# Kernel optimization log

Hardware: AMD Instinct MI355X
Metric: run time of the kernel (lower is better)

The kernel has to match this reference:

```python
import jax, jax.numpy as jnp
import numpy as np
import math

DIM = 96
NUM_HEADS = 8
MLP_RATIO = 4.0

def _coord_encoding(h, w, scale, d_model):
    # matches HierarchicalCoordinateEncoding: per freq i, channels are
    # [sin(cell_y), cos(cell_y), sin(cell_x), cos(cell_x), sin(y), cos(y), sin(x), cos(x)]
    y = jnp.arange(h, dtype=jnp.float32) / (h - 1)
    x = jnp.arange(w, dtype=jnp.float32) / (w - 1)
    yy, xx = jnp.meshgrid(y, x, indexing='ij')
    yf = yy.reshape(-1)
    xf = xx.reshape(-1)
    cs = 2.0 / scale
    coords4 = jnp.stack([yf * cs, xf * cs, yf, xf], axis=-1)  # [N,4]
    nf = d_model // 8
    freqs = (2.0 ** jnp.arange(nf, dtype=jnp.float32)) * math.pi  # [nf]
    phase = coords4[:, None, :] * freqs[None, :, None]  # [N,nf,4]
    enc = jnp.stack([jnp.sin(phase), jnp.cos(phase)], axis=-1)  # [N,nf,4,2]
    return enc.reshape(h * w, nf * 8)  # [N,d_model] (d_model divisible by 8)

def _layernorm(x, g, b, eps=1e-5):
    mu = jnp.mean(x, axis=-1, keepdims=True)
    var = jnp.var(x, axis=-1, keepdims=True)
    return (x - mu) * jax.lax.rsqrt(var + eps) * g + b

def setup_inputs():
    key = jax.random.key(0)
    ks = jax.random.split(key, 8)
    B, C, H, W = 8, DIM, 96, 96
    hid = int(DIM * MLP_RATIO)
    std = 0.02
    return {
        'features': jax.random.normal(ks[0], (B, C, H, W), jnp.float32),
        'scale': 2,
        'mlp1_w1': jax.random.normal(ks[1], (2 * DIM, hid), jnp.float32) * std,
        'mlp1_b1': jnp.zeros((hid,), jnp.float32),
        'mlp1_w2': jax.random.normal(ks[2], (hid, DIM), jnp.float32) * std,
        'mlp1_b2': jnp.zeros((DIM,), jnp.float32),
        'norm1_g': jnp.ones((DIM,), jnp.float32),
        'norm1_b': jnp.zeros((DIM,), jnp.float32),
        'qkv_w': jax.random.normal(ks[3], (DIM, 3 * DIM), jnp.float32) * std,
        'proj_w': jax.random.normal(ks[4], (DIM, DIM), jnp.float32) * std,
        'proj_b': jnp.zeros((DIM,), jnp.float32),
        'norm2_g': jnp.ones((DIM,), jnp.float32),
        'norm2_b': jnp.zeros((DIM,), jnp.float32),
        'mlp2_w1': jax.random.normal(ks[5], (DIM, hid), jnp.float32) * std,
        'mlp2_b1': jnp.zeros((hid,), jnp.float32),
        'mlp2_w2': jax.random.normal(ks[6], (hid, 3), jnp.float32) * std,
        'mlp2_b2': jnp.zeros((3,), jnp.float32),
    }

def reference(features, scale, mlp1_w1, mlp1_b1, mlp1_w2, mlp1_b2, norm1_g, norm1_b, qkv_w, proj_w, proj_b, norm2_g, norm2_b, mlp2_w1, mlp2_b1, mlp2_w2, mlp2_b2):
    B, C, H_lr, W_lr = features.shape
    H, W = int(H_lr * scale), int(W_lr * scale)
    N = H * W
    nh = NUM_HEADS
    hd = C // nh
    ce = _coord_encoding(H, W, float(scale), C)  # [N,C]
    # bilinear upsample, half-pixel centers == torch align_corners=False
    feat_up = jax.image.resize(features, (B, C, H, W), method='linear')
    feat_flat = feat_up.transpose(0, 2, 3, 1).reshape(B, N, C)
    combined = jnp.concatenate([feat_flat, jnp.broadcast_to(ce[None], (B, N, C))], axis=-1)  # [B,N,2C]
    x = jax.nn.gelu(combined @ mlp1_w1 + mlp1_b1, approximate=False) @ mlp1_w2 + mlp1_b2  # [B,N,C]
    x = _layernorm(x, norm1_g, norm1_b)
    # linear attention: softmax over q feature dim and k token dim
    qkv = (x @ qkv_w).reshape(B, N, 3, nh, hd).transpose(2, 0, 3, 1, 4)  # [3,B,nh,N,hd]
    q, k, v = qkv[0], qkv[1], qkv[2]
    q = jax.nn.softmax(q, axis=-1) * (hd ** -0.5)
    k = jax.nn.softmax(k, axis=-2)
    ctx = jnp.einsum('bhnd,bhne->bhde', k, v)  # [B,nh,hd,hd]
    attn = jnp.einsum('bhnd,bhde->bhne', q, ctx)  # [B,nh,N,hd]
    attn = attn.transpose(0, 2, 1, 3).reshape(B, N, C)
    x = x + (attn @ proj_w + proj_b)
    x = _layernorm(x, norm2_g, norm2_b)
    rgb = jax.nn.gelu(x @ mlp2_w1 + mlp2_b1, approximate=False) @ mlp2_w2 + mlp2_b2  # [B,N,3]
    rgb = rgb.reshape(B, H, W, 3).transpose(0, 3, 1, 2)  # [B,3,H,W]
    return jnp.clip(jnp.tanh(rgb) * 0.5 + 0.5, 0.0, 1.0)
```

## Files before the change

kernel.cpp:

```cpp
#include <hip/hip_runtime.h>
#include <math.h>

typedef unsigned short u16;
typedef unsigned int   u32;
typedef unsigned long long u64;
typedef __bf16  bf16x8 __attribute__((ext_vector_type(8)));
typedef short   s16x8  __attribute__((ext_vector_type(8)));
typedef float   f32x4  __attribute__((ext_vector_type(4)));

#define NTOK 36864
#define TTOT (8*NTOK)

__device__ __forceinline__ f32x4 mfma16(s16x8 a, s16x8 b, f32x4 c){
  return __builtin_amdgcn_mfma_f32_16x16x32_bf16(
      __builtin_bit_cast(bf16x8, a), __builtin_bit_cast(bf16x8, b), c, 0, 0, 0);
}
__device__ __forceinline__ int swz(int row, int bc, int stride){
  return row*stride + (bc ^ ((row&7)<<4));
}
__device__ __forceinline__ u16 f2bf(float f){
  u32 u = __float_as_uint(f);
  return (u16)((u + 0x7fffu + ((u>>16)&1u)) >> 16);
}
__device__ __forceinline__ u32 pk2f(float a, float b){
  return (u32)f2bf(a) | ((u32)f2bf(b)<<16);
}
__device__ __forceinline__ u64 pk4f(float a, float b, float c, float d){
  return (u64)pk2f(a,b) | ((u64)pk2f(c,d)<<32);
}
__device__ __forceinline__ float bf2f(u16 h){ return __uint_as_float(((u32)h)<<16); }
__device__ __forceinline__ float rcp_(float x){ return __builtin_amdgcn_rcpf(x); }

__device__ __forceinline__ float gelu_(float x){
  float z = fabsf(x) * 0.70710678118654752f;
  float t = rcp_(1.0f + 0.3275911f*z);
  float poly = t*(0.254829592f + t*(-0.284496736f + t*(1.421413741f + t*(-1.453152027f + t*1.061405429f))));
  float e = __expf(-z*z);
  float erf = 1.0f - poly*e;
  erf = (x < 0.0f) ? -erf : erf;
  return 0.5f*x*(1.0f + erf);
}
__device__ __forceinline__ float tanhf_(float x){
  float e = __expf(2.0f*x);
  return 1.0f - 2.0f*rcp_(e + 1.0f);
}

#define LDSF(arr, row, kc, stride) (*(const s16x8*)((const char*)(arr) + swz((row),(kc)*2,(stride))))

__global__ void prep_w(const float* __restrict__ w1, const float* __restrict__ w2,
                       const float* __restrict__ qkvw, const float* __restrict__ projw,
                       const float* __restrict__ m2w1, const float* __restrict__ m2w2,
                       u16* __restrict__ w1t, u16* __restrict__ w2t,
                       u16* __restrict__ wqt, u16* __restrict__ wkt, u16* __restrict__ wvt,
                       u16* __restrict__ pjt, u16* __restrict__ m2w1t, u16* __restrict__ m2w2t)
{
  int i = blockIdx.x*256 + threadIdx.x;
  if (i < 73728){ int n=i/192, k=i%192; w1t[i] = f2bf(w1[k*384+n]); return; }
  i -= 73728;
  if (i < 36864){ int n=i/384, k=i%384; w2t[i] = f2bf(w2[k*96+n]); return; }
  i -= 36864;
  if (i < 9216){ int n=i/96, k=i%96; wqt[i] = f2bf(qkvw[k*288+n]); return; }
  i -= 9216;
  if (i < 9216){ int n=i/96, k=i%96; wkt[i] = f2bf(qkvw[k*288+96+n]); return; }
  i -= 9216;
  if (i < 9216){ int n=i/96, k=i%96; wvt[i] = f2bf(qkvw[k*288+192+n]); return; }
  i -= 9216;
  if (i < 9216){ int n=i/96, k=i%96; pjt[i] = f2bf(projw[k*96+n]); return; }
  i -= 9216;
  if (i < 36864){ int n=i/96, k=i%96; m2w1t[i] = f2bf(m2w1[k*384+n]); return; }
  i -= 36864;
  if (i < 6144){ int n=i/384, k=i%384; m2w2t[i] = (n<3)? f2bf(m2w2[k*3+n]) : (u16)0; return; }
}

__global__ void prep_feat(const float* __restrict__ feat, u16* __restrict__ featcl){
  __shared__ u16 t[96*100];
  const int tid = threadIdx.x;
  const int b = blockIdx.x/96, y = blockIdx.x%96;
  for (int i=tid; i<9216; i+=256){
    int c = i/96, x = i%96;
    t[c*100+x] = f2bf(feat[((size_t)(b*96+c)*96 + y)*96 + x]);
  }
  __syncthreads();
  for (int i=tid; i<9216; i+=256){
    int x = i/96, c = i%96;
    featcl[(((size_t)b*96 + y)*96 + x)*96 + c] = t[c*100+x];
  }
}

__global__ void prep_ce(u16* __restrict__ ce){
  int gid = blockIdx.x*256 + threadIdx.x;
  if (gid >= 36864*48) return;
  int n = gid/48, c2 = gid%48;
  int row = n/192, col = n%192;
  int fi = c2>>2, cs = c2&3;
  float coord = ((cs&1)==0) ? (float)row*(1.0f/191.0f) : (float)col*(1.0f/191.0f);
  float u = coord * (float)(1<<fi);
  u = u - 2.0f*floorf(u*0.5f);
  float ph = u * 3.14159265358979323846f;
  float s, c;
  __sincosf(ph, &s, &c);
  *(u32*)(ce + (size_t)n*96 + c2*2) = pk2f(s, c);
}

__global__ __launch_bounds__(256,3) void k1(
    const u16* __restrict__ featcl, const u16* __restrict__ ce,
    const u16* __restrict__ w1t, const float* __restrict__ b1,
    const u16* __restrict__ w2t, const float* __restrict__ b2,
    const float* __restrict__ g1, const float* __restrict__ be1,
    const u16* __restrict__ wkt, const u16* __restrict__ wvt,
    u16* __restrict__ x1, float* __restrict__ ctx_un)
{
  __shared__ u16 comb[64*192];
  __shared__ char scratch[26624];
  const int tid = threadIdx.x, w = tid>>6, lane = tid&63, kg = lane>>4, ln = lane&15;
  const int bi = blockIdx.x;
  const int b = bi/576, rem = bi%576, ty = rem/24, tx = rem%24;
  u16* hid  = (u16*)scratch;
  u16* ektp = (u16*)scratch;
  u16* vtp  = (u16*)(scratch + 12288);

  for (int i=tid; i<1024; i+=256){
    int rr = 96 + (i>>6), t = i&63;
    *(u16*)((char*)vtp + swz(rr, t*2, 128)) = (rr==96) ? (u16)0x3f80 : (u16)0;
  }

  {
    const u16* fbase = featcl + (size_t)b*884736;
    const int l = tid>>2, cg = tid&3;
    int row = ty*8 + (l>>3), col = tx*8 + (l&7);
    int y0 = (row-1)>>1;
    int y0c = max(y0,0), y1c = min(y0+1,95);
    float wy1 = (row&1) ? 0.25f : 0.75f;
    float wy0 = 1.0f - wy1;
    int x0 = (col-1)>>1;
    int x0c = max(x0,0), x1c = min(x0+1,95);
    float wx1 = (col&1) ? 0.25f : 0.75f;
    float wx0 = 1.0f - wx1;
    float w00=wy0*wx0, w01=wy0*wx1, w10=wy1*wx0, w11=wy1*wx1;
    const u16* p00 = fbase + (size_t)(y0c*96+x0c)*96 + cg*24;
    const u16* p01 = fbase + (size_t)(y0c*96+x1c)*96 + cg*24;
    const u16* p10 = fbase + (size_t)(y1c*96+x0c)*96 + cg*24;
    const u16* p11 = fbase + (size_t)(y1c*96+x1c)*96 + cg*24;
    #pragma unroll
    for (int g=0; g<3; ++g){
      s16x8 v00 = *(const s16x8*)(p00 + g*8);
      s16x8 v01 = *(const s16x8*)(p01 + g*8);
      s16x8 v10 = *(const s16x8*)(p10 + g*8);
      s16x8 v11 = *(const s16x8*)(p11 + g*8);
      #pragma unroll
      for (int j2=0; j2<4; ++j2){
        u32 u00 = ((const u32*)&v00)[j2], u01 = ((const u32*)&v01)[j2];
        u32 u10 = ((const u32*)&v10)[j2], u11 = ((const u32*)&v11)[j2];
        float a0 = w00*bf2f((u16)u00) + w01*bf2f((u16)u01)
                 + w10*bf2f((u16)u10) + w11*bf2f((u16)u11);
        float a1 = w00*bf2f((u16)(u00>>16)) + w01*bf2f((u16)(u01>>16))
                 + w10*bf2f((u16)(u10>>16)) + w11*bf2f((u16)(u11>>16));
        *(u32*)((char*)comb + swz(l, (cg*24 + g*8 + j2*2)*2, 384)) = pk2f(a0, a1);
      }
    }
  }
  for (int i=tid; i<64*12; i+=256){
    int l = i/12, sg = i%12;
    int n = (ty*8+(l>>3))*192 + tx*8 + (l&7);
    *(s16x8*)((char*)comb + swz(l, 192 + sg*16, 384)) = *(const s16x8*)(ce + (size_t)n*96 + sg*8);
  }
  __syncthreads();

  f32x4 a2[6] = {};
  for (int h=0; h<2; ++h){
    f32x4 acc[3][4] = {};
    #pragma unroll
    for (int ks=0; ks<6; ++ks){
      s16x8 af[3];
      #pragma unroll
      for (int nf=0; nf<3; ++nf)
        af[nf] = *(const s16x8*)(w1t + (size_t)(192*h+48*w+16*nf+ln)*192 + ks*32+8*kg);
      #pragma unroll
      for (int tf=0; tf<4; ++tf){
        s16x8 bfr = LDSF(comb, 16*tf+ln, ks*32+8*kg, 384);
        #pragma unroll
        for (int nf=0; nf<3; ++nf) acc[nf][tf] = mfma16(af[nf], bfr, acc[nf][tf]);
      }
    }
    #pragma unroll
    for (int nf=0; nf<3; ++nf){
      int lc0 = 48*w + 16*nf + 4*kg;
      float4 bb = *(const float4*)(b1 + 192*h + lc0);
      #pragma unroll
      for (int tf=0; tf<4; ++tf){
        int token = 16*tf + ln;
        u64 v = pk4f(gelu_(acc[nf][tf][0]+bb.x), gelu_(acc[nf][tf][1]+bb.y),
                     gelu_(acc[nf][tf][2]+bb.z), gelu_(acc[nf][tf][3]+bb.w));
        *(u64*)((char*)hid + swz(token, lc0*2, 384)) = v;
      }
    }
    __syncthreads();
    #pragma unroll
    for (int ks=0; ks<6; ++ks){
      s16x8 af = LDSF(hid, 16*w+ln, ks*32+8*kg, 384);
      #pragma unroll
      for (int nf=0; nf<6; ++nf){
        s16x8 bfr = *(const s16x8*)(w2t + (size_t)(16*nf+ln)*384 + 192*h + ks*32+8*kg);
        a2[nf] = mfma16(af, bfr, a2[nf]);
      }
    }
    if (h==0) __syncthreads();
  }

  float gg[6], bbv[6];
  #pragma unroll
  for (int nf=0; nf<6; ++nf){
    int col = 16*nf + ln;
    float bias = b2[col];
    gg[nf] = g1[col]; bbv[nf] = be1[col];
    #pragma unroll
    for (int r=0; r<4; ++r) a2[nf][r] += bias;
  }
  __syncthreads();
  #pragma unroll
  for (int r=0; r<4; ++r){
    float s=0.f, sq=0.f;
    #pragma unroll
    for (int nf=0; nf<6; ++nf){ float v=a2[nf][r]; s+=v; sq+=v*v; }
    #pragma unroll
    for (int m=8; m; m>>=1){ s += __shfl_xor(s,m); sq += __shfl_xor(sq,m); }
    float mean = s*(1.f/96.f);
    float var  = sq*(1.f/96.f) - mean*mean;
    float rstd = rsqrtf(var + 1e-5f);
    int trow = 16*w + 4*kg + r;
    #pragma unroll
    for (int nf=0; nf<6; ++nf){
      float o = (a2[nf][r]-mean)*rstd*gg[nf] + bbv[nf];
      *(u16*)((char*)comb + swz(trow, (16*nf+ln)*2, 256)) = f2bf(o);
    }
  }
  __syncthreads();

  for (int i=tid; i<64*12; i+=256){
    int l = i/12, sg = i%12;
    s16x8 v = *(const s16x8*)((const char*)comb + swz(l, sg*16, 256));
    int n = (ty*8+(l>>3))*192 + tx*8 + (l&7);
    *(s16x8*)(x1 + ((size_t)b*NTOK + n)*96 + sg*8) = v;
  }

  {
    f32x4 ka[6] = {}, va[6] = {};
    #pragma unroll
    for (int ks=0; ks<3; ++ks){
      s16x8 xb = LDSF(comb, 16*w+ln, ks*32+8*kg, 256);
      #pragma unroll
      for (int mf=0; mf<6; ++mf){
        s16x8 ak = *(const s16x8*)(wkt + (size_t)(16*mf+ln)*96 + ks*32+8*kg);
        s16x8 av = *(const s16x8*)(wvt + (size_t)(16*mf+ln)*96 + ks*32+8*kg);
        ka[mf] = mfma16(ak, xb, ka[mf]);
        va[mf] = mfma16(av, xb, va[mf]);
      }
    }
    #pragma unroll
    for (int mf=0; mf<6; ++mf){
      #pragma unroll
      for (int r=0; r<4; ++r){
        int d = 16*mf + 4*kg + r;
        int tok = 16*w + ln;
        *(u16*)((char*)ektp + swz(d, tok*2, 128)) = f2bf(__expf(ka[mf][r]));
        *(u16*)((char*)vtp  + swz(d, tok*2, 128)) = f2bf(va[mf][r]);
      }
    }
  }
  __syncthreads();

  {
    const int tmi[20] = {0,0,1,1,1,2,2,3,3,4,4,4,5,5, 0,1,2,3,4,5};
    const int tni[20] = {0,1,0,1,2,1,2,3,4,3,4,5,4,5, 6,6,6,6,6,6};
    f32x4 c5[5] = {};
    #pragma unroll
    for (int t=0; t<20; ++t){
      if (t/5 == w){
        #pragma unroll
        for (int grp=0; grp<2; ++grp){
          s16x8 ea = LDSF(ektp, 16*tmi[t]+ln, 32*grp+8*kg, 128);
          s16x8 vb = LDSF(vtp,  16*tni[t]+ln, 32*grp+8*kg, 128);
          c5[t%5] = mfma16(ea, vb, c5[t%5]);
        }
      }
    }
    #pragma unroll
    for (int t=0; t<20; ++t){
      if (t/5 == w){
        #pragma unroll
        for (int r=0; r<4; ++r){
          int d = 16*tmi[t] + 4*kg + r;
          if (tni[t]==6){
            if (ln==0) atomicAdd(&ctx_un[(b*96+d)*112 + 96], c5[t%5][r]);
          } else {
            int e = 16*tni[t] + ln;
            if (d/12 == e/12) atomicAdd(&ctx_un[(b*96+d)*112 + e], c5[t%5][r]);
          }
        }
      }
    }
  }
}

__global__ void k2c(const float* __restrict__ ctx_un, u16* __restrict__ ctxBG){
  int i = blockIdx.x*256 + threadIdx.x;
  if (i >= 8*112*128) return;
  int b = i/14336, rr = i%14336, row = rr/128, d = rr%128;
  u16 v = 0;
  if (row < 96){
    if (d < 96 && d/12 == row/12){
      float c = ctx_un[(b*96+d)*112 + row] / ctx_un[(b*96+d)*112 + 96];
      v = f2bf(c * 0.28867513459481287f);
    }
  } else {
    int h = row - 96;
    if (d < 96 && d/12 == h) v = (u16)0x3f80;
  }
  ctxBG[(size_t)b*14336 + row*128 + d] = v;
}

__global__ __launch_bounds__(256,2) void k3(
    const u16* __restrict__ x1, const u16* __restrict__ wqt, const u16* __restrict__ ctxBG,
    const u16* __restrict__ pjt,
    const float* __restrict__ projb, const float* __restrict__ g2, const float* __restrict__ be2,
    const u16* __restrict__ m2w1t, const float* __restrict__ m2b1,
    const u16* __restrict__ m2w2t, const float* __restrict__ m2b2,
    float* __restrict__ out)
{
  __shared__ u16 bufA[128*128];
  __shared__ u16 bufB[128*128];
  __shared__ float rgbsh[3][128];
  const int tid = threadIdx.x, w = tid>>6, lane = tid&63, kg = lane>>4, ln = lane&15;
  const int bi = blockIdx.x, b = bi/288;
  const size_t t0 = (size_t)bi*128;
  const int n0 = (bi%288)*128;

  {
    s16x8 wq[18], xbv[6];
    #pragma unroll
    for (int ks=0; ks<3; ++ks)
      #pragma unroll
      for (int nf=0; nf<6; ++nf)
        wq[ks*6+nf] = *(const s16x8*)(wqt + (size_t)(16*nf+ln)*96 + ks*32+8*kg);
    #pragma unroll
    for (int tf=0; tf<2; ++tf)
      #pragma unroll
      for (int ks=0; ks<3; ++ks)
        xbv[tf*3+ks] = *(const s16x8*)(x1 + (t0 + 32*w + 16*tf + ln)*96 + ks*32+8*kg);
    f32x4 q[6][2] = {};
    #pragma unroll
    for (int ks=0; ks<3; ++ks)
      #pragma unroll
      for (int tf=0; tf<2; ++tf)
        #pragma unroll
        for (int nf=0; nf<6; ++nf)
          q[nf][tf] = mfma16(wq[ks*6+nf], xbv[tf*3+ks], q[nf][tf]);
    #pragma unroll
    for (int nf=0; nf<6; ++nf){
      #pragma unroll
      for (int tf=0; tf<2; ++tf){
        int token = 32*w + 16*tf + ln;
        u64 v = pk4f(__expf(q[nf][tf][0]), __expf(q[nf][tf][1]),
                     __expf(q[nf][tf][2]), __expf(q[nf][tf][3]));
        *(u64*)((char*)bufA + swz(token, (16*nf+4*kg)*2, 256)) = v;
      }
    }
  }

  f32x4 p[2][7] = {};
  {
    const u16* cb = ctxBG + (size_t)b*14336;
    s16x8 cbf[21];
    #pragma unroll
    for (int ks=0; ks<3; ++ks)
      #pragma unroll
      for (int nf=0; nf<7; ++nf)
        cbf[ks*7+nf] = *(const s16x8*)(cb + (size_t)(16*nf+ln)*128 + ks*32+8*kg);
    #pragma unroll
    for (int ks=0; ks<3; ++ks){
      s16x8 a[2];
      #pragma unroll
      for (int mi=0; mi<2; ++mi) a[mi] = LDSF(bufA, 16*(2*w+mi)+ln, ks*32+8*kg, 256);
      #pragma unroll
      for (int nf=0; nf<7; ++nf){
        #pragma unroll
        for (int mi=0; mi<2; ++mi) p[mi][nf] = mfma16(a[mi], cbf[ks*7+nf], p[mi][nf]);
      }
    }
  }
  f32x4 pp[2][6];
  #pragma unroll
  for (int mi=0; mi<2; ++mi)
    #pragma unroll
    for (int nf=0; nf<6; ++nf)
      #pragma unroll
      for (int r=0; r<4; ++r)
        pp[mi][nf][r] = bf2f(x1[(t0 + 16*(2*w+mi)+4*kg+r)*96 + 16*nf+ln]);
  s16x8 pjf[18];
  #pragma unroll
  for (int ks=0; ks<3; ++ks)
    #pragma unroll
    for (int nf=0; nf<6; ++nf)
      pjf[ks*6+nf] = *(const s16x8*)(pjt + (size_t)(16*nf+ln)*96 + ks*32+8*kg);
  #pragma unroll
  for (int mi=0; mi<2; ++mi){
    f32x4 inv;
    #pragma unroll
    for (int r=0; r<4; ++r) inv[r] = rcp_(p[mi][6][r]);
    #pragma unroll
    for (int nf=0; nf<6; ++nf){
      int h = (16*nf + ln) / 12;
      int src = (lane & 0x30) + h;
      #pragma unroll
      for (int r=0; r<4; ++r){
        float iv = __shfl(inv[r], src, 64);
        int trow = 16*(2*w+mi) + 4*kg + r;
        *(u16*)((char*)bufB + swz(trow, (16*nf+ln)*2, 256)) = f2bf(p[mi][nf][r] * iv);
      }
    }
  }

  #pragma unroll
  for (int ks=0; ks<3; ++ks){
    s16x8 a[2];
    #pragma unroll
    for (int mi=0; mi<2; ++mi) a[mi] = LDSF(bufB, 16*(2*w+mi)+ln, ks*32+8*kg, 256);
    #pragma unroll
    for (int nf=0; nf<6; ++nf){
      #pragma unroll
      for (int mi=0; mi<2; ++mi) pp[mi][nf] = mfma16(a[mi], pjf[ks*6+nf], pp[mi][nf]);
    }
  }
  {
    float gg[6], bbv[6], pb[6];
    #pragma unroll
    for (int nf=0; nf<6; ++nf){
      int col = 16*nf + ln;
      pb[nf] = projb[col]; gg[nf] = g2[col]; bbv[nf] = be2[col];
    }
    #pragma unroll
    for (int mi=0; mi<2; ++mi){
      #pragma unroll
      for (int r=0; r<4; ++r){
        int trow = 16*(2*w+mi)+4*kg+r;
        float vv[6]; float s=0.f, sq=0.f;
        #pragma unroll
        for (int nf=0; nf<6; ++nf){
          float v = pp[mi][nf][r] + pb[nf];
          vv[nf] = v; s += v; sq += v*v;
        }
        #pragma unroll
        for (int m=8; m; m>>=1){ s += __shfl_xor(s,m); sq += __shfl_xor(sq,m); }
        float mean = s*(1.f/96.f);
        float var  = sq*(1.f/96.f) - mean*mean;
        float rstd = rsqrtf(var + 1e-5f);
        #pragma unroll
        for (int nf=0; nf<6; ++nf){
          float o = (vv[nf]-mean)*rstd*gg[nf] + bbv[nf];
          *(u16*)((char*)bufA + swz(trow, (16*nf+ln)*2, 256)) = f2bf(o);
        }
      }
    }
  }

  f32x4 rgb[2] = {};
  for (int nc=0; nc<4; ++nc){
    s16x8 wm[18];
    #pragma unroll
    for (int ks=0; ks<3; ++ks)
      #pragma unroll
      for (int nf=0; nf<6; ++nf)
        wm[ks*6+nf] = *(const s16x8*)(m2w1t + (size_t)(nc*96+16*nf+ln)*96 + ks*32+8*kg);
    s16x8 wv2[3];
    #pragma unroll
    for (int ks=0; ks<3; ++ks)
      wv2[ks] = *(const s16x8*)(m2w2t + (size_t)ln*384 + nc*96 + ks*32 + 8*kg);
    f32x4 hh[6][2] = {};
    #pragma unroll
    for (int ks=0; ks<3; ++ks){
      #pragma unroll
      for (int tf=0; tf<2; ++tf){
        s16x8 bfr = LDSF(bufA, 32*w+16*tf+ln, ks*32+8*kg, 256);
        #pragma unroll
        for (int nf=0; nf<6; ++nf) hh[nf][tf] = mfma16(wm[ks*6+nf], bfr, hh[nf][tf]);
      }
    }
    #pragma unroll
    for (int nf=0; nf<6; ++nf){
      int hc0 = nc*96 + 16*nf + 4*kg;
      float4 bb = *(const float4*)(m2b1 + hc0);
      #pragma unroll
      for (int tf=0; tf<2; ++tf){
        int token = 32*w + 16*tf + ln;
        u64 v = pk4f(gelu_(hh[nf][tf][0]+bb.x), gelu_(hh[nf][tf][1]+bb.y),
                     gelu_(hh[nf][tf][2]+bb.z), gelu_(hh[nf][tf][3]+bb.w));
        *(u64*)((char*)bufB + swz(token, (16*nf+4*kg)*2, 256)) = v;
      }
    }
    #pragma unroll
    for (int ks=0; ks<3; ++ks){
      #pragma unroll
      for (int mi=0; mi<2; ++mi){
        s16x8 a = LDSF(bufB, 16*(2*w+mi)+ln, ks*32+8*kg, 256);
        rgb[mi] = mfma16(a, wv2[ks], rgb[mi]);
      }
    }
  }
  if (ln < 3){
    float bias = m2b2[ln];
    #pragma unroll
    for (int mi=0; mi<2; ++mi)
      #pragma unroll
      for (int r=0; r<4; ++r){
        int trow = 16*(2*w+mi)+4*kg+r;
        float v = tanhf_(rgb[mi][r] + bias)*0.5f + 0.5f;
        v = fminf(fmaxf(v, 0.f), 1.f);
        rgbsh[ln][trow] = v;
      }
  }
  __syncthreads();
  for (int i=tid; i<384; i+=256){
    int ch = i>>7, t = i&127;
    out[((size_t)(b*3+ch))*NTOK + n0 + t] = rgbsh[ch][t];
  }
}

extern "C" void kernel_launch(void* const* d_in, const int* in_sizes, int n_in,
                              void* d_out, int out_size, void* d_ws, size_t ws_size,
                              hipStream_t stream)
{
  (void)in_sizes; (void)n_in; (void)out_size; (void)ws_size;
  const float* feat  = (const float*)d_in[0];
  const float* m1w1  = (const float*)d_in[2];
  const float* m1b1  = (const float*)d_in[3];
  const float* m1w2  = (const float*)d_in[4];
  const float* m1b2  = (const float*)d_in[5];
  const float* n1g   = (const float*)d_in[6];
  const float* n1b   = (const float*)d_in[7];
  const float* qkvw  = (const float*)d_in[8];
  const float* projw = (const float*)d_in[9];
  const float* projb = (const float*)d_in[10];
  const float* n2g   = (const float*)d_in[11];
  const float* n2b   = (const float*)d_in[12];
  const float* m2w1  = (const float*)d_in[13];
  const float* m2b1  = (const float*)d_in[14];
  const float* m2w2  = (const float*)d_in[15];
  const float* m2b2  = (const float*)d_in[16];
  float* out = (float*)d_out;

  char* p = (char*)d_ws;
  auto bump = [&](size_t bytes)->char*{
    char* r = p;
    p += (bytes + 255) & ~(size_t)255;
    return r;
  };
  u16*  x1     = (u16*) bump((size_t)TTOT*96*2);
  u16*  featcl = (u16*) bump((size_t)8*96*96*96*2);
  u16*  ce     = (u16*) bump((size_t)NTOK*96*2);
  u16*  w1t    = (u16*) bump(73728*2);
  u16*  w2t    = (u16*) bump(36864*2);
  u16*  wqt    = (u16*) bump(9216*2);
  u16*  wkt    = (u16*) bump(9216*2);
  u16*  wvt    = (u16*) bump(9216*2);
  u16*  pjt    = (u16*) bump(9216*2);
  u16*  m2w1t  = (u16*) bump(36864*2);
  u16*  m2w2t  = (u16*) bump(6144*2);
  float* ctx_un= (float*)bump((size_t)8*96*112*4);
  u16*  ctxBG  = (u16*) bump((size_t)8*112*128*2);

  hipLaunchKernelGGL(prep_w, dim3(744), dim3(256), 0, stream,
                     m1w1, m1w2, qkvw, projw, m2w1, m2w2,
                     w1t, w2t, wqt, wkt, wvt, pjt, m2w1t, m2w2t);
  hipLaunchKernelGGL(prep_feat, dim3(768), dim3(256), 0, stream, feat, featcl);
  hipLaunchKernelGGL(prep_ce, dim3(6912), dim3(256), 0, stream, ce);
  hipMemsetAsync(ctx_un, 0, (size_t)8*96*112*4, stream);
  hipLaunchKernelGGL(k1, dim3(4608), dim3(256), 0, stream,
                     featcl, ce, w1t, m1b1, w2t, m1b2, n1g, n1b, wkt, wvt, x1, ctx_un);
  hipLaunchKernelGGL(k2c, dim3(448), dim3(256), 0, stream, ctx_un, ctxBG);
  hipLaunchKernelGGL(k3, dim3(2304), dim3(256), 0, stream,
                     x1, wqt, ctxBG, pjt, projb, n2g, n2b, m2w1t, m2b1, m2w2t, m2b2, out);
}
```

Before: 483.2 us.

## Compute full MLP1 hidden layer in one pass with 32x32 MFMA tiles

The first MLP layer now computes all 384 hidden channels at once with 32x32x16 MFMA instructions, storing the whole 64x384 hidden tile in a larger LDS buffer instead of two 192-channel halves. The second GEMM then runs once over K=384, which removes the half-loop and a barrier, and the vtp constant-row initialization moves to after the scratch region is no longer in use. The larger LDS footprint lowers occupancy, and the launch bound drops from 3 to 2 blocks per SM to match. The aim is fewer barriers and better MFMA efficiency at the cost of less latency hiding.

```diff
diff --git a/kernel.cpp b/kernel.cpp
--- a/kernel.cpp
+++ b/kernel.cpp
@@ -7,12 +7,17 @@
 typedef __bf16  bf16x8 __attribute__((ext_vector_type(8)));
 typedef short   s16x8  __attribute__((ext_vector_type(8)));
 typedef float   f32x4  __attribute__((ext_vector_type(4)));
+typedef float   f32x16 __attribute__((ext_vector_type(16)));
 
 #define NTOK 36864
 #define TTOT (8*NTOK)
 
 __device__ __forceinline__ f32x4 mfma16(s16x8 a, s16x8 b, f32x4 c){
   return __builtin_amdgcn_mfma_f32_16x16x32_bf16(
+      __builtin_bit_cast(bf16x8, a), __builtin_bit_cast(bf16x8, b), c, 0, 0, 0);
+}
+__device__ __forceinline__ f32x16 mfma32(s16x8 a, s16x8 b, f32x16 c){
+  return __builtin_amdgcn_mfma_f32_32x32x16_bf16(
       __builtin_bit_cast(bf16x8, a), __builtin_bit_cast(bf16x8, b), c, 0, 0, 0);
 }
 __device__ __forceinline__ int swz(int row, int bc, int stride){
@@ -102,7 +107,7 @@
   *(u32*)(ce + (size_t)n*96 + c2*2) = pk2f(s, c);
 }
 
-__global__ __launch_bounds__(256,3) void k1(
+__global__ __launch_bounds__(256,2) void k1(
     const u16* __restrict__ featcl, const u16* __restrict__ ce,
     const u16* __restrict__ w1t, const float* __restrict__ b1,
     const u16* __restrict__ w2t, const float* __restrict__ b2,
@@ -111,18 +116,13 @@
     u16* __restrict__ x1, float* __restrict__ ctx_un)
 {
   __shared__ u16 comb[64*192];
-  __shared__ char scratch[26624];
+  __shared__ u16 hid[64*384];
   const int tid = threadIdx.x, w = tid>>6, lane = tid&63, kg = lane>>4, ln = lane&15;
+  const int l31 = lane&31, kh = lane>>5;
   const int bi = blockIdx.x;
   const int b = bi/576, rem = bi%576, ty = rem/24, tx = rem%24;
-  u16* hid  = (u16*)scratch;
-  u16* ektp = (u16*)scratch;
-  u16* vtp  = (u16*)(scratch + 12288);
-
-  for (int i=tid; i<1024; i+=256){
-    int rr = 96 + (i>>6), t = i&63;
-    *(u16*)((char*)vtp + swz(rr, t*2, 128)) = (rr==96) ? (u16)0x3f80 : (u16)0;
-  }
+  u16* ektp = hid;
+  u16* vtp  = (u16*)((char*)hid + 12288);
 
   {
     const u16* fbase = featcl + (size_t)b*884736;
@@ -166,47 +166,49 @@
   }
   __syncthreads();
 
+  {
+    f32x16 acc[3][2] = {};
+    #pragma unroll
+    for (int ks=0; ks<12; ++ks){
+      s16x8 af[3];
+      #pragma unroll
+      for (int tt=0; tt<3; ++tt)
+        af[tt] = *(const s16x8*)(w1t + (size_t)(96*w + 32*tt + l31)*192 + ks*16 + 8*kh);
+      #pragma unroll
+      for (int tk=0; tk<2; ++tk){
+        s16x8 bfr = LDSF(comb, 32*tk + l31, ks*16 + 8*kh, 384);
+        #pragma unroll
+        for (int tt=0; tt<3; ++tt) acc[tt][tk] = mfma32(af[tt], bfr, acc[tt][tk]);
+      }
+    }
+    #pragma unroll
+    for (int tt=0; tt<3; ++tt){
+      #pragma unroll
+      for (int g=0; g<4; ++g){
+        int hc0 = 96*w + 32*tt + 8*g + 4*kh;
+        float4 bb = *(const float4*)(b1 + hc0);
+        #pragma unroll
+        for (int tk=0; tk<2; ++tk){
+          int token = 32*tk + l31;
+          u64 v = pk4f(gelu_(acc[tt][tk][4*g+0]+bb.x), gelu_(acc[tt][tk][4*g+1]+bb.y),
+                       gelu_(acc[tt][tk][4*g+2]+bb.z), gelu_(acc[tt][tk][4*g+3]+bb.w));
+          *(u64*)((char*)hid + swz(token, hc0*2, 768)) = v;
+        }
+      }
+    }
+  }
+  __syncthreads();
+
   f32x4 a2[6] = {};
-  for (int h=0; h<2; ++h){
-    f32x4 acc[3][4] = {};
-    #pragma unroll
-    for (int ks=0; ks<6; ++ks){
-      s16x8 af[3];
-      #pragma unroll
-      for (int nf=0; nf<3; ++nf)
-        af[nf] = *(const s16x8*)(w1t + (size_t)(192*h+48*w+16*nf+ln)*192 + ks*32+8*kg);
-      #pragma unroll
-      for (int tf=0; tf<4; ++tf){
-        s16x8 bfr = LDSF(comb, 16*tf+ln, ks*32+8*kg, 384);
-        #pragma unroll
-        for (int nf=0; nf<3; ++nf) acc[nf][tf] = mfma16(af[nf], bfr, acc[nf][tf]);
-      }
-    }
-    #pragma unroll
-    for (int nf=0; nf<3; ++nf){
-      int lc0 = 48*w + 16*nf + 4*kg;
-      float4 bb = *(const float4*)(b1 + 192*h + lc0);
-      #pragma unroll
-      for (int tf=0; tf<4; ++tf){
-        int token = 16*tf + ln;
-        u64 v = pk4f(gelu_(acc[nf][tf][0]+bb.x), gelu_(acc[nf][tf][1]+bb.y),
-                     gelu_(acc[nf][tf][2]+bb.z), gelu_(acc[nf][tf][3]+bb.w));
-        *(u64*)((char*)hid + swz(token, lc0*2, 384)) = v;
-      }
-    }
-    __syncthreads();
-    #pragma unroll
-    for (int ks=0; ks<6; ++ks){
-      s16x8 af = LDSF(hid, 16*w+ln, ks*32+8*kg, 384);
-      #pragma unroll
-      for (int nf=0; nf<6; ++nf){
-        s16x8 bfr = *(const s16x8*)(w2t + (size_t)(16*nf+ln)*384 + 192*h + ks*32+8*kg);
-        a2[nf] = mfma16(af, bfr, a2[nf]);
-      }
-    }
-    if (h==0) __syncthreads();
-  }
-
+  #pragma unroll
+  for (int ks=0; ks<12; ++ks){
+    s16x8 afr = LDSF(hid, 16*w+ln, ks*32+8*kg, 768);
+    #pragma unroll
+    for (int nf=0; nf<6; ++nf){
+      s16x8 bfr = *(const s16x8*)(w2t + (size_t)(16*nf+ln)*384 + ks*32+8*kg);
+      a2[nf] = mfma16(afr, bfr, a2[nf]);
+    }
+  }
   float gg[6], bbv[6];
   #pragma unroll
   for (int nf=0; nf<6; ++nf){
@@ -216,7 +218,6 @@
     #pragma unroll
     for (int r=0; r<4; ++r) a2[nf][r] += bias;
   }
-  __syncthreads();
   #pragma unroll
   for (int r=0; r<4; ++r){
     float s=0.f, sq=0.f;
@@ -235,6 +236,11 @@
     }
   }
   __syncthreads();
+
+  for (int i=tid; i<1024; i+=256){
+    int rr = 96 + (i>>6), t = i&63;
+    *(u16*)((char*)vtp + swz(rr, t*2, 128)) = (rr==96) ? (u16)0x3f80 : (u16)0;
+  }
 
   for (int i=tid; i<64*12; i+=256){
     int l = i/12, sg = i%12;
```

Result: slower. 495.4 us (+2.5%).
